# Optimization experiments

Measured on AMD Instinct MI355X. Metric: run time of the kernel, lower is better.

The kernel has to match this reference:

```python
import jax, jax.numpy as jnp
import numpy as np

N_HEADS = 4

def _conv2d(x, w, b):
    # NCHW input, OIHW weight, 3x3 SAME, stride 1
    y = jax.lax.conv_general_dilated(x, w, window_strides=(1, 1), padding='SAME',
                                     dimension_numbers=('NCHW', 'OIHW', 'NCHW'))
    return y + b[None, :, None, None]


def setup_inputs() -> dict:
    key = jax.random.key(0)
    ks = jax.random.split(key, 5)
    x = jax.random.normal(ks[0], (4, 32, 256, 256), dtype=jnp.float32)
    conv1_w = jax.random.normal(ks[1], (384, 32, 3, 3), dtype=jnp.float32) * 0.05
    conv1_b = jax.random.normal(ks[2], (384,), dtype=jnp.float32) * 0.05
    conv2_w = jax.random.normal(ks[3], (32, 128, 3, 3), dtype=jnp.float32) * 0.05
    conv2_b = jax.random.normal(ks[4], (32,), dtype=jnp.float32) * 0.05
    return {'x': x, 'conv1_w': conv1_w, 'conv1_b': conv1_b,
            'conv2_w': conv2_w, 'conv2_b': conv2_b}


def reference(x, conv1_w, conv1_b, conv2_w, conv2_b):
    b, c_in, h, w = x.shape
    n = h * w
    qkv = _conv2d(x, conv1_w, conv1_b)              # [b, 3*heads*d, h, w]
    d = qkv.shape[1] // (3 * N_HEADS)               # head dim
    qkv = qkv.reshape(b, 3, N_HEADS, d, n)          # 'b (qkv heads c) h w -> b qkv heads c n'
    q, k, v = qkv[:, 0], qkv[:, 1], qkv[:, 2]
    k = jax.nn.softmax(k, axis=-1)                  # softmax over n = h*w
    weights = jnp.einsum('bhdn,bhen->bhde', q, k)   # [b, heads, d, d] context
    out = jnp.einsum('bhde,bhdn->bhen', weights, v) # [b, heads, d, n]
    out = out.reshape(b, N_HEADS * d, h, w)         # 'b heads c n -> b (heads c) h w'
    return _conv2d(out, conv2_w, conv2_b)
```

## Files before the change

### kernel.cpp

```cpp
#include <hip/hip_runtime.h>
#include <hip/hip_bf16.h>

typedef __hip_bfloat16 bf16;
typedef __attribute__((ext_vector_type(8))) short short8;
typedef __attribute__((ext_vector_type(4))) float f32x4;
typedef __attribute__((ext_vector_type(16))) float f32x16;

#define B_    4
#define CIN   32
#define HH    256
#define WW    256
#define C1    384
#define NPIX  65536
#define CMID  128
#define COUT  32
#define PW    258
#define VROW  16512

static __device__ __forceinline__ float u2f(unsigned short u) {
    unsigned int x = ((unsigned int)u) << 16;
    return __uint_as_float(x);
}
static __device__ __forceinline__ unsigned short f2u(float f) {
    bf16 h = __float2bfloat16(f);
    return __builtin_bit_cast(unsigned short, h);
}
static __device__ __forceinline__ unsigned int pk2(float lo, float hi) {
    return (unsigned int)f2u(lo) | ((unsigned int)f2u(hi) << 16);
}
static __device__ __forceinline__ void gload16(const void* src, void* dst) {
    __builtin_amdgcn_global_load_lds(
        (const __attribute__((address_space(1))) void*)src,
        (__attribute__((address_space(3))) void*)dst, 16, 0, 0);
}

__global__ __launch_bounds__(256) void k_w1t(const float* __restrict__ w1, short* __restrict__ w1t) {
    const int tap = blockIdx.x;
    for (int i = threadIdx.x; i < 384 * 32; i += 256) {
        int co = i >> 5, cij = i & 31;
        w1t[((size_t)(tap * 4 + (cij >> 3)) * 384 + co) * 8 + (cij & 7)] =
            (short)f2u(w1[(size_t)i * 9 + tap]);
    }
}

__global__ __launch_bounds__(256) void k_xt2(const float* __restrict__ x,
                                             unsigned short* __restrict__ xt2, int b0) {
    const int row = blockIdx.x, bl = blockIdx.y, b = b0 + bl;
    const int tx = threadIdx.x;
    unsigned short* rbase = xt2 + (size_t)(bl * PW + row) * 4 * PW * 8;
    const uint4 z = make_uint4(0u, 0u, 0u, 0u);
    if (row == 0 || row == PW - 1) {
        for (int i = tx; i < 4 * PW; i += 256) ((uint4*)rbase)[i] = z;
        return;
    }
    if (tx < 2) {
        int c = tx ? (PW - 1) : 0;
#pragma unroll
        for (int ch = 0; ch < 4; ch++)
            *(uint4*)(rbase + ((size_t)ch * PW + c) * 8) = z;
    }
    const int col = tx + 1;
    const size_t px = (size_t)(row - 1) * WW + tx;
    unsigned int pk[16];
#pragma unroll
    for (int c2 = 0; c2 < 16; c2++) {
        float v0 = x[((size_t)b * CIN + 2 * c2) * NPIX + px];
        float v1 = x[((size_t)b * CIN + 2 * c2 + 1) * NPIX + px];
        pk[c2] = pk2(v0, v1);
    }
#pragma unroll
    for (int ch = 0; ch < 4; ch++)
        *(uint4*)(rbase + ((size_t)ch * PW + col) * 8) =
            make_uint4(pk[ch * 4], pk[ch * 4 + 1], pk[ch * 4 + 2], pk[ch * 4 + 3]);
}

__global__ __launch_bounds__(256) void k_bordv(unsigned short* __restrict__ vt) {
    const int row = blockIdx.x, bp = blockIdx.y, tx = threadIdx.x;
    unsigned short* base = vt + ((size_t)bp * PW + row) * VROW;
    const uint4 z = make_uint4(0u, 0u, 0u, 0u);
    if (row == 0 || row == PW - 1) {
        for (int i = tx; i < VROW / 8; i += 256) ((uint4*)base)[i] = z;
    } else if (tx < 16) {
        int g = tx >> 1, c = (tx & 1) * (PW - 1);
        *(uint4*)(base + ((size_t)g * PW + c) * 8) = z;
    }
}

__global__ __launch_bounds__(256, 3) void k_conv1(
    const unsigned short* __restrict__ xt2, const short* __restrict__ w1t,
    const float* __restrict__ b1, unsigned short* __restrict__ vt,
    unsigned short* __restrict__ pw, float* __restrict__ ps, int nb)
{
    const int nblk = 512 * nb;
    const int m = ((int)blockIdx.x & 7) * (nblk >> 3) + ((int)blockIdx.x >> 3);
    const int chunk = m & 1;
    const int y   = (m >> 1) & 255;
    const int bl  = m >> 9;
    const int px0 = chunk * 128;
    const int cid = bl * 512 + y * 2 + chunk;
    const int tx  = threadIdx.x;
    const int wv  = tx >> 6, l = tx & 63;
    const int lhi = l >> 4, llo = l & 15;

    __shared__ short xs[12 * 132 * 8];
    __shared__ union {
        short os[64][136];
        short ost[128][66];
        short osw[4][32][32];
    } ou;

#pragma unroll
    for (int i = 0; i < 3; i++) {
        int p = wv * 3 + i;
        int r = p >> 2, ch = p & 3;
        const char* src = (const char*)xt2 +
            (((size_t)(bl * PW) + y + r) * 4 + ch) * (PW * 16) + (size_t)px0 * 16 + (size_t)l * 16;
        char* dst = (char*)xs + p * 2112;
        gload16(src, dst);
        gload16(src + 1024, dst + 1024);
        if (l < 2) gload16(src + 2048, dst + 2048);
    }
    __syncthreads();

    const short* wbase = w1t + ((size_t)lhi * 384 + llo) * 8;

    short8 qa[2][4];
    f32x4 wacc[2][2];
#pragma unroll
    for (int dt = 0; dt < 2; dt++)
#pragma unroll
        for (int et = 0; et < 2; et++) wacc[dt][et] = (f32x4){0.f, 0.f, 0.f, 0.f};
    float se0 = 0.f, se1 = 0.f;

#pragma unroll
    for (int cog = 0; cog < 6; cog++) {
        const int co0 = cog * 64;

        f32x4 acc[2][4];
#pragma unroll
        for (int t = 0; t < 2; t++)
#pragma unroll
            for (int mc = 0; mc < 4; mc++) acc[t][mc] = (f32x4){0.f, 0.f, 0.f, 0.f};

        short8 a[4], an[4];
#pragma unroll
        for (int mc = 0; mc < 4; mc++)
            an[mc] = *(const short8*)(wbase + ((size_t)co0 + mc * 16) * 8);
#pragma unroll
        for (int tap = 0; tap < 9; tap++) {
            const int dy = tap / 3, dx = tap % 3;
#pragma unroll
            for (int mc = 0; mc < 4; mc++) a[mc] = an[mc];
            if (tap < 8) {
#pragma unroll
                for (int mc = 0; mc < 4; mc++)
                    an[mc] = *(const short8*)(wbase +
                        ((size_t)(tap + 1) * 4 * 384 + co0 + mc * 16) * 8);
            }
#pragma unroll
            for (int t = 0; t < 2; t++) {
                short8 bfr = *(const short8*)&xs[(((dy * 4 + lhi) * 132) + (wv * 32 + t * 16 + llo + dx)) * 8];
#pragma unroll
                for (int mc = 0; mc < 4; mc++)
                    acc[t][mc] = __builtin_amdgcn_mfma_f32_16x16x32_bf16(a[mc], bfr, acc[t][mc], 0, 0, 0);
            }
        }

        float bias[4][4];
#pragma unroll
        for (int mc = 0; mc < 4; mc++)
#pragma unroll
            for (int r = 0; r < 4; r++)
                bias[mc][r] = b1[co0 + mc * 16 + lhi * 4 + r];

        __syncthreads();

        if (cog < 4) {
#pragma unroll
            for (int t = 0; t < 2; t++)
#pragma unroll
                for (int mc = 0; mc < 4; mc++)
#pragma unroll
                    for (int r = 0; r < 4; r++)
                        ou.os[mc * 16 + lhi * 4 + r][wv * 32 + t * 16 + llo] =
                            (short)f2u(acc[t][mc][r] + bias[mc][r]);
        } else {
#pragma unroll
            for (int t = 0; t < 2; t++)
#pragma unroll
                for (int mc = 0; mc < 4; mc++)
#pragma unroll
                    for (int r = 0; r < 4; r++)
                        ou.ost[wv * 32 + t * 16 + llo][mc * 16 + lhi * 4 + r] =
                            (short)f2u(acc[t][mc][r] + bias[mc][r]);
        }
        __syncthreads();

        if (cog < 2) {
            if ((wv >> 1) == cog) {
                const int chb = (wv & 1) * 32;
#pragma unroll
                for (int dt = 0; dt < 2; dt++)
#pragma unroll
                    for (int ks = 0; ks < 4; ks++)
                        qa[dt][ks] = *(const short8*)&ou.os[chb + dt * 16 + llo][ks * 32 + lhi * 8];
            }
        } else if (cog < 4) {
            if ((wv >> 1) == cog - 2) {
                const int chb = (wv & 1) * 32;
#pragma unroll
                for (int et = 0; et < 2; et++)
#pragma unroll
                    for (int ks = 0; ks < 4; ks++) {
                        short8 kf = *(const short8*)&ou.os[chb + et * 16 + llo][ks * 32 + lhi * 8];
                        short8 pf;
#pragma unroll
                        for (int j = 0; j < 8; j++) {
                            float ef = __expf(u2f((unsigned short)kf[j]));
                            if (et == 0) se0 += ef; else se1 += ef;
                            pf[j] = (short)f2u(ef);
                        }
#pragma unroll
                        for (int dt = 0; dt < 2; dt++)
                            wacc[dt][et] = __builtin_amdgcn_mfma_f32_16x16x32_bf16(
                                qa[dt][ks], pf, wacc[dt][et], 0, 0, 0);
                    }
            }
        } else {
            const int plane = cog - 4;
            unsigned short* rowb = vt + ((size_t)(bl * 2 + plane) * PW + 1 + y) * VROW;
#pragma unroll
            for (int i = 0; i < 4; i++) {
                int u = i * 256 + tx;
                int g = u >> 7, px = u & 127;
                uint4 v = *(const uint4*)&ou.ost[px][g * 8];
                *(uint4*)(rowb + ((size_t)g * PW + 1 + px0 + px) * 8) = v;
            }
        }
    }

    se0 += __shfl_xor(se0, 16); se0 += __shfl_xor(se0, 32);
    se1 += __shfl_xor(se1, 16); se1 += __shfl_xor(se1, 32);
    if (l < 16) {
        ps[(size_t)cid * 128 + wv * 32 + llo]      = se0;
        ps[(size_t)cid * 128 + wv * 32 + 16 + llo] = se1;
    }

    __syncthreads();
#pragma unroll
    for (int dt = 0; dt < 2; dt++)
#pragma unroll
        for (int et = 0; et < 2; et++)
#pragma unroll
            for (int r = 0; r < 4; r++)
                ou.osw[wv][dt * 16 + lhi * 4 + r][et * 16 + llo] = (short)f2u(wacc[dt][et][r]);
    __syncthreads();

    {
        unsigned short* pwp = pw + (size_t)cid * 4096;
        const unsigned short* osf = (const unsigned short*)&ou;
#pragma unroll
        for (int p = 0; p < 2; p++)
            *(uint4*)(pwp + p * 2048 + tx * 8) = *(const uint4*)(osf + p * 2048 + tx * 8);
    }
}

__global__ __launch_bounds__(256) void k_wred(
    const unsigned short* __restrict__ pw, const float* __restrict__ ps,
    float* __restrict__ wts, int b0)
{
    const int bh = blockIdx.x;
    const int jq = blockIdx.y;
    const int bl = bh >> 2, h = bh & 3;
    const int tx = threadIdx.x;
    __shared__ float rinvs[32];
    if (tx < 32) {
        float s = 0.f;
        const float* pp = ps + (size_t)bl * 512 * 128 + h * 32 + tx;
        for (int c = 0; c < 512; c++) s += pp[(size_t)c * 128];
        rinvs[tx] = 1.f / s;
    }
    __syncthreads();
    const int i = jq * 256 + tx;
    const unsigned short* pwp = pw + (size_t)bl * 512 * 4096 + h * 1024 + i;
    float s = 0.f;
    for (int c = 0; c < 512; c++) s += u2f(pwp[(size_t)c * 4096]);
    wts[(size_t)(b0 * 4 + bh) * 1024 + i] = s * rinvs[i & 31];
}

__global__ __launch_bounds__(256) void k_w2e(
    const float* __restrict__ w2, const float* __restrict__ wts,
    short* __restrict__ w2te, int b0)
{
    const int bl = blockIdx.x, tap = blockIdx.y;
    const int tx = threadIdx.x;
    __shared__ float Wsh[4096];
    __shared__ float w2sh[4096];
    for (int i = tx; i < 4096; i += 256) {
        Wsh[i]  = wts[(size_t)(b0 + bl) * 4096 + i];
        w2sh[i] = w2[(size_t)i * 9 + tap];
    }
    __syncthreads();
#pragma unroll
    for (int rep = 0; rep < 16; rep++) {
        int o = rep * 256 + tx;
        int cv = o >> 5, co = o & 31;
        int h = cv >> 5, d = cv & 31;
        const float* wp = &w2sh[co * 128 + 32 * h];
        const float* Wp = &Wsh[h * 1024 + d * 32];
        float s = 0.f;
#pragma unroll
        for (int e = 0; e < 32; e++) s += wp[e] * Wp[e];
        w2te[((((size_t)bl * 9 + tap) * 16 + (cv >> 3)) * 32 + co) * 8 + (cv & 7)] =
            (short)f2u(s);
    }
}

__global__ __launch_bounds__(256, 3) void k_conv2e(
    const unsigned short* __restrict__ vt, const short* __restrict__ w2te,
    const float* __restrict__ b2, float* __restrict__ out, int b0, int nb)
{
    const int nblk = 512 * nb;
    const int m = ((int)blockIdx.x & 7) * (nblk >> 3) + ((int)blockIdx.x >> 3);
    const int chunk = m & 1;
    const int y   = (m >> 1) & 255;
    const int bl  = m >> 9;
    const int px0 = chunk * 128;
    const int bb  = b0 + bl;
    const int tx  = threadIdx.x;
    const int wv  = tx >> 6, l = tx & 63;
    const int lhi = l >> 4, llo = l & 15;

    __shared__ short xs[12 * 132 * 8];
    __shared__ float osf[32][132];

    const short* w2b = w2te + (size_t)bl * 9 * 16 * 32 * 8;

    float bias[2][4];
#pragma unroll
    for (int mm = 0; mm < 2; mm++)
#pragma unroll
        for (int r = 0; r < 4; r++)
            bias[mm][r] = b2[mm * 16 + lhi * 4 + r];

    f32x4 acc[2][2];
#pragma unroll
    for (int t = 0; t < 2; t++)
#pragma unroll
        for (int mm = 0; mm < 2; mm++) acc[t][mm] = (f32x4){0.f, 0.f, 0.f, 0.f};

    for (int cc = 0; cc < 4; cc++) {
        const int plane = cc >> 1, ghalf = cc & 1;
        __syncthreads();
#pragma unroll
        for (int i = 0; i < 3; i++) {
            int p = wv * 3 + i;
            int r = p >> 2, sg = p & 3;
            const char* src = (const char*)vt +
                (((size_t)(bl * 2 + plane) * PW + y + r) * VROW
                 + ((size_t)(ghalf * 4 + sg) * PW + px0) * 8) * 2 + (size_t)l * 16;
            char* dst = (char*)xs + p * 2112;
            gload16(src, dst);
            gload16(src + 1024, dst + 1024);
            if (l < 2) gload16(src + 2048, dst + 2048);
        }
        __syncthreads();

        short8 a[2], an[2];
#pragma unroll
        for (int mm = 0; mm < 2; mm++)
            an[mm] = *(const short8*)(w2b + ((size_t)(cc * 4 + lhi) * 32 + mm * 16 + llo) * 8);
#pragma unroll
        for (int tap = 0; tap < 9; tap++) {
            const int dy = tap / 3, dx = tap % 3;
#pragma unroll
            for (int mm = 0; mm < 2; mm++) a[mm] = an[mm];
            if (tap < 8) {
#pragma unroll
                for (int mm = 0; mm < 2; mm++)
                    an[mm] = *(const short8*)(w2b +
                        ((size_t)((tap + 1) * 16 + cc * 4 + lhi) * 32 + mm * 16 + llo) * 8);
            }
#pragma unroll
            for (int t = 0; t < 2; t++) {
                short8 bfr = *(const short8*)&xs[(((dy * 4 + lhi) * 132) + (wv * 32 + t * 16 + llo + dx)) * 8];
#pragma unroll
                for (int mm = 0; mm < 2; mm++)
                    acc[t][mm] = __builtin_amdgcn_mfma_f32_16x16x32_bf16(a[mm], bfr, acc[t][mm], 0, 0, 0);
            }
        }
    }

#pragma unroll
    for (int t = 0; t < 2; t++)
#pragma unroll
        for (int mm = 0; mm < 2; mm++)
#pragma unroll
            for (int r = 0; r < 4; r++)
                osf[mm * 16 + lhi * 4 + r][wv * 32 + t * 16 + llo] = acc[t][mm][r] + bias[mm][r];
    __syncthreads();
#pragma unroll
    for (int p = 0; p < 4; p++) {
        int chl = p * 8 + (tx >> 5);
        float4 v = *(const float4*)&osf[chl][(tx & 31) * 4];
        *(float4*)(out + ((size_t)bb * COUT + chl) * NPIX + y * WW + px0 + (tx & 31) * 4) = v;
    }
}

extern "C" void kernel_launch(void* const* d_in, const int* in_sizes, int n_in,
                              void* d_out, int out_size, void* d_ws, size_t ws_size,
                              hipStream_t stream) {
    const float* x  = (const float*)d_in[0];
    const float* w1 = (const float*)d_in[1];
    const float* b1 = (const float*)d_in[2];
    const float* w2 = (const float*)d_in[3];
    const float* b2 = (const float*)d_in[4];
    float* out = (float*)d_out;

    char* ws = (char*)d_ws;
    float* wts  = (float*)(ws + 4096);
    short* w1t  = (short*)(ws + 69632);
    short* w2te = (short*)(ws + 364544);
    const size_t OFF_XT = 1048576;

    int nb = 4;
    size_t xt_sz = (size_t)nb * PW * 4 * PW * 16;
    size_t pw_sz = (size_t)nb * 512 * 4096 * 2;
    size_t ps_sz = (size_t)nb * 512 * 128 * 4;
    size_t vt_sz = (size_t)nb * 2 * PW * (size_t)VROW * 2;
    if (ws_size < OFF_XT + xt_sz + pw_sz + ps_sz + vt_sz) {
        nb = 1;
        xt_sz = (size_t)nb * PW * 4 * PW * 16;
        pw_sz = (size_t)nb * 512 * 4096 * 2;
        ps_sz = (size_t)nb * 512 * 128 * 4;
        vt_sz = (size_t)nb * 2 * PW * (size_t)VROW * 2;
    }
    const size_t pw_off = OFF_XT + xt_sz;
    const size_t ps_off = pw_off + pw_sz;
    const size_t vt_off = ps_off + ps_sz;

    unsigned short* xt2 = (unsigned short*)(ws + OFF_XT);
    unsigned short* pw  = (unsigned short*)(ws + pw_off);
    float*          psb = (float*)(ws + ps_off);
    unsigned short* vt  = (unsigned short*)(ws + vt_off);

    k_w1t<<<dim3(9), 256, 0, stream>>>(w1, w1t);

    for (int b0 = 0; b0 < B_; b0 += nb) {
        k_xt2  <<<dim3(PW, nb),      256, 0, stream>>>(x, xt2, b0);
        k_bordv<<<dim3(PW, nb * 2),  256, 0, stream>>>(vt);
        k_conv1<<<dim3(2 * HH * nb), 256, 0, stream>>>(xt2, w1t, b1, vt, pw, psb, nb);
        k_wred <<<dim3(nb * 4, 4),   256, 0, stream>>>(pw, psb, wts, b0);
        k_w2e  <<<dim3(nb, 9),       256, 0, stream>>>(w2, wts, w2te, b0);
        k_conv2e<<<dim3(2 * HH * nb),256, 0, stream>>>(vt, w2te, b2, out, b0, nb);
    }
}
```

Before: 197.2 us.

## Double-buffer LDS staging in conv1 output and conv2 input tiles

In k_conv1, the shared output staging buffer becomes two buffers that alternate per channel group. This removes the barrier before each write and the one before the final weights write. In k_conv2e, the input tile is double-buffered so the next channel chunk's global-to-LDS loads are issued before computing on the current chunk. The larger LDS footprint comes with launch bounds lowered from 3 to 2 blocks per CU, which cuts occupancy in exchange for overlap.

Result: faster. 186.7 us (-5.3%).

```diff
diff --git a/kernel.cpp b/kernel.cpp
--- a/kernel.cpp
+++ b/kernel.cpp
@@ -86,7 +86,7 @@
     }
 }
 
-__global__ __launch_bounds__(256, 3) void k_conv1(
+__global__ __launch_bounds__(256, 2) void k_conv1(
     const unsigned short* __restrict__ xt2, const short* __restrict__ w1t,
     const float* __restrict__ b1, unsigned short* __restrict__ vt,
     unsigned short* __restrict__ pw, float* __restrict__ ps, int nb)
@@ -103,11 +103,12 @@
     const int lhi = l >> 4, llo = l & 15;
 
     __shared__ short xs[12 * 132 * 8];
-    __shared__ union {
+    union obuf {
         short os[64][136];
         short ost[128][66];
         short osw[4][32][32];
-    } ou;
+    };
+    __shared__ obuf ou2[2];
 
 #pragma unroll
     for (int i = 0; i < 3; i++) {
@@ -135,6 +136,7 @@
 #pragma unroll
     for (int cog = 0; cog < 6; cog++) {
         const int co0 = cog * 64;
+        const int p   = cog & 1;
 
         f32x4 acc[2][4];
 #pragma unroll
@@ -173,8 +175,6 @@
             for (int r = 0; r < 4; r++)
                 bias[mc][r] = b1[co0 + mc * 16 + lhi * 4 + r];
 
-        __syncthreads();
-
         if (cog < 4) {
 #pragma unroll
             for (int t = 0; t < 2; t++)
@@ -182,7 +182,7 @@
                 for (int mc = 0; mc < 4; mc++)
 #pragma unroll
                     for (int r = 0; r < 4; r++)
-                        ou.os[mc * 16 + lhi * 4 + r][wv * 32 + t * 16 + llo] =
+                        ou2[p].os[mc * 16 + lhi * 4 + r][wv * 32 + t * 16 + llo] =
                             (short)f2u(acc[t][mc][r] + bias[mc][r]);
         } else {
 #pragma unroll
@@ -191,7 +191,7 @@
                 for (int mc = 0; mc < 4; mc++)
 #pragma unroll
                     for (int r = 0; r < 4; r++)
-                        ou.ost[wv * 32 + t * 16 + llo][mc * 16 + lhi * 4 + r] =
+                        ou2[p].ost[wv * 32 + t * 16 + llo][mc * 16 + lhi * 4 + r] =
                             (short)f2u(acc[t][mc][r] + bias[mc][r]);
         }
         __syncthreads();
@@ -203,7 +203,7 @@
                 for (int dt = 0; dt < 2; dt++)
 #pragma unroll
                     for (int ks = 0; ks < 4; ks++)
-                        qa[dt][ks] = *(const short8*)&ou.os[chb + dt * 16 + llo][ks * 32 + lhi * 8];
+                        qa[dt][ks] = *(const short8*)&ou2[p].os[chb + dt * 16 + llo][ks * 32 + lhi * 8];
             }
         } else if (cog < 4) {
             if ((wv >> 1) == cog - 2) {
@@ -212,7 +212,7 @@
                 for (int et = 0; et < 2; et++)
 #pragma unroll
                     for (int ks = 0; ks < 4; ks++) {
-                        short8 kf = *(const short8*)&ou.os[chb + et * 16 + llo][ks * 32 + lhi * 8];
+                        short8 kf = *(const short8*)&ou2[p].os[chb + et * 16 + llo][ks * 32 + lhi * 8];
                         short8 pf;
 #pragma unroll
                         for (int j = 0; j < 8; j++) {
@@ -233,7 +233,7 @@
             for (int i = 0; i < 4; i++) {
                 int u = i * 256 + tx;
                 int g = u >> 7, px = u & 127;
-                uint4 v = *(const uint4*)&ou.ost[px][g * 8];
+                uint4 v = *(const uint4*)&ou2[p].ost[px][g * 8];
                 *(uint4*)(rowb + ((size_t)g * PW + 1 + px0 + px) * 8) = v;
             }
         }
@@ -246,22 +246,21 @@
         ps[(size_t)cid * 128 + wv * 32 + 16 + llo] = se1;
     }
 
-    __syncthreads();
 #pragma unroll
     for (int dt = 0; dt < 2; dt++)
 #pragma unroll
         for (int et = 0; et < 2; et++)
 #pragma unroll
             for (int r = 0; r < 4; r++)
-                ou.osw[wv][dt * 16 + lhi * 4 + r][et * 16 + llo] = (short)f2u(wacc[dt][et][r]);
+                ou2[0].osw[wv][dt * 16 + lhi * 4 + r][et * 16 + llo] = (short)f2u(wacc[dt][et][r]);
     __syncthreads();
 
     {
         unsigned short* pwp = pw + (size_t)cid * 4096;
-        const unsigned short* osf = (const unsigned short*)&ou;
-#pragma unroll
-        for (int p = 0; p < 2; p++)
-            *(uint4*)(pwp + p * 2048 + tx * 8) = *(const uint4*)(osf + p * 2048 + tx * 8);
+        const unsigned short* osf = (const unsigned short*)&ou2[0];
+#pragma unroll
+        for (int p2 = 0; p2 < 2; p2++)
+            *(uint4*)(pwp + p2 * 2048 + tx * 8) = *(const uint4*)(osf + p2 * 2048 + tx * 8);
     }
 }
 
@@ -316,7 +315,7 @@
     }
 }
 
-__global__ __launch_bounds__(256, 3) void k_conv2e(
+__global__ __launch_bounds__(256, 2) void k_conv2e(
     const unsigned short* __restrict__ vt, const short* __restrict__ w2te,
     const float* __restrict__ b2, float* __restrict__ out, int b0, int nb)
 {
@@ -331,7 +330,7 @@
     const int wv  = tx >> 6, l = tx & 63;
     const int lhi = l >> 4, llo = l & 15;
 
-    __shared__ short xs[12 * 132 * 8];
+    __shared__ short xs2[2][12 * 132 * 8];
     __shared__ float osf[32][132];
 
     const short* w2b = w2te + (size_t)bl * 9 * 16 * 32 * 8;
@@ -349,23 +348,40 @@
 #pragma unroll
         for (int mm = 0; mm < 2; mm++) acc[t][mm] = (f32x4){0.f, 0.f, 0.f, 0.f};
 
+#pragma unroll
+    for (int i = 0; i < 3; i++) {
+        int p = wv * 3 + i;
+        int r = p >> 2, sg = p & 3;
+        const char* src = (const char*)vt +
+            (((size_t)(bl * 2 + 0) * PW + y + r) * VROW
+             + ((size_t)(0 * 4 + sg) * PW + px0) * 8) * 2 + (size_t)l * 16;
+        char* dst = (char*)xs2[0] + p * 2112;
+        gload16(src, dst);
+        gload16(src + 1024, dst + 1024);
+        if (l < 2) gload16(src + 2048, dst + 2048);
+    }
+
+#pragma unroll
     for (int cc = 0; cc < 4; cc++) {
-        const int plane = cc >> 1, ghalf = cc & 1;
         __syncthreads();
-#pragma unroll
-        for (int i = 0; i < 3; i++) {
-            int p = wv * 3 + i;
-            int r = p >> 2, sg = p & 3;
-            const char* src = (const char*)vt +
-                (((size_t)(bl * 2 + plane) * PW + y + r) * VROW
-                 + ((size_t)(ghalf * 4 + sg) * PW + px0) * 8) * 2 + (size_t)l * 16;
-            char* dst = (char*)xs + p * 2112;
-            gload16(src, dst);
-            gload16(src + 1024, dst + 1024);
-            if (l < 2) gload16(src + 2048, dst + 2048);
+
+        if (cc < 3) {
+            const int nplane = (cc + 1) >> 1, nghalf = (cc + 1) & 1;
+#pragma unroll
+            for (int i = 0; i < 3; i++) {
+                int p = wv * 3 + i;
+                int r = p >> 2, sg = p & 3;
+                const char* src = (const char*)vt +
+                    (((size_t)(bl * 2 + nplane) * PW + y + r) * VROW
+                     + ((size_t)(nghalf * 4 + sg) * PW + px0) * 8) * 2 + (size_t)l * 16;
+                char* dst = (char*)xs2[(cc + 1) & 1] + p * 2112;
+                gload16(src, dst);
+                gload16(src + 1024, dst + 1024);
+                if (l < 2) gload16(src + 2048, dst + 2048);
+            }
         }
-        __syncthreads();
-
+
+        const short* xsc = xs2[cc & 1];
         short8 a[2], an[2];
 #pragma unroll
         for (int mm = 0; mm < 2; mm++)
@@ -383,7 +399,7 @@
             }
 #pragma unroll
             for (int t = 0; t < 2; t++) {
-                short8 bfr = *(const short8*)&xs[(((dy * 4 + lhi) * 132) + (wv * 32 + t * 16 + llo + dx)) * 8];
+                short8 bfr = *(const short8*)&xsc[(((dy * 4 + lhi) * 132) + (wv * 32 + t * 16 + llo + dx)) * 8];
 #pragma unroll
                 for (int mm = 0; mm < 2; mm++)
                     acc[t][mm] = __builtin_amdgcn_mfma_f32_16x16x32_bf16(a[mm], bfr, acc[t][mm], 0, 0, 0);
@@ -391,6 +407,7 @@
         }
     }
 
+    __syncthreads();
 #pragma unroll
     for (int t = 0; t < 2; t++)
 #pragma unroll
```
